# Performance work log

Measured on AMD Instinct MI355X. Metric: run time of the kernel, lower is better.

## Reference

```python
import jax, jax.numpy as jnp
import numpy as np

N_NODES = 100000
N_EDGES = 3200000
IN_DIM = 3
HID = 8
OUT_DIM = 1


def setup_inputs() -> dict:
    key = jax.random.key(0)
    ks = jax.random.split(key, 10)
    x = jax.random.normal(ks[0], (N_NODES, IN_DIM), dtype=jnp.float32)
    edge_index = jax.random.randint(ks[1], (2, N_EDGES), 0, N_NODES, dtype=jnp.int64)
    cat_dim = 2 * (HID + IN_DIM)  # 22
    s = lambda fan_in: 1.0 / np.sqrt(fan_in)
    W_in = jax.random.uniform(ks[2], (IN_DIM, HID), jnp.float32, -s(IN_DIM), s(IN_DIM))
    b_in = jnp.zeros((HID,), jnp.float32)
    W1 = jax.random.uniform(ks[3], (cat_dim, HID), jnp.float32, -s(cat_dim), s(cat_dim))
    b1 = jnp.zeros((HID,), jnp.float32)
    W2 = jax.random.uniform(ks[4], (HID, HID), jnp.float32, -s(HID), s(HID))
    b2 = jnp.zeros((HID,), jnp.float32)
    W_e = jax.random.uniform(ks[5], (cat_dim, OUT_DIM), jnp.float32, -s(cat_dim), s(cat_dim))
    b_e = jnp.zeros((OUT_DIM,), jnp.float32)
    return {"x": x, "edge_index": edge_index, "W_in": W_in, "b_in": b_in,
            "W1": W1, "b1": b1, "W2": W2, "b2": b2, "W_e": W_e, "b_e": b_e}


def reference(x, edge_index, W_in, b_in, W1, b1, W2, b2, W_e, b_e):
    src = edge_index[0]  # j (source)
    dst = edge_index[1]  # i (target)

    # inputnet: Linear + Tanh
    H = jnp.tanh(x @ W_in + b_in)               # [N, HID]
    feat = jnp.concatenate([H, x], axis=-1)      # [N, HID+IN_DIM]

    # One EdgeConv iteration (n_iters=1): message = nn(cat([x_i, x_j - x_i]))
    xi = feat[dst]                                # [E, 11]
    xj = feat[src]                                # [E, 11]
    e = jnp.concatenate([xi, xj - xi], axis=-1)   # [E, 22]
    m = jax.nn.sigmoid(e @ W1 + b1)               # [E, HID]
    m = jax.nn.sigmoid(m @ W2 + b2)               # [E, HID]
    H = jax.ops.segment_sum(m, dst, num_segments=N_NODES)  # scatter-add to targets
    feat = jnp.concatenate([H, x], axis=-1)       # [N, 11]

    # edgenetwork on concatenated endpoint features
    ef = jnp.concatenate([feat[src], feat[dst]], axis=-1)   # [E, 22]
    out = jax.nn.sigmoid(ef @ W_e + b_e)          # [E, 1]
    return out.squeeze(-1)                        # [E]
```

## Files before the change

kernel.cpp:

```cpp
#include <hip/hip_runtime.h>
#include <hip/hip_fp16.h>

#define TPB     256
#define BSH     9
#define BW      512
#define EPB     8192
#define NBMAX   256
#define MAXNB   1024
#define S_SPLIT 8
#define FXS     2097152.0f
#define FXSI    (1.0f / 2097152.0f)

static __device__ __forceinline__ float sigmoidf(float v) {
    return __builtin_amdgcn_rcpf(1.0f + __expf(-v));
}

static __device__ __forceinline__ void unpack8(uint4 u, float o[8]) {
    union { unsigned int u; __half2 h; } c0, c1, c2, c3;
    c0.u = u.x; c1.u = u.y; c2.u = u.z; c3.u = u.w;
    float2 f0 = __half22float2(c0.h), f1 = __half22float2(c1.h);
    float2 f2 = __half22float2(c2.h), f3 = __half22float2(c3.h);
    o[0]=f0.x; o[1]=f0.y; o[2]=f1.x; o[3]=f1.y;
    o[4]=f2.x; o[5]=f2.y; o[6]=f3.x; o[7]=f3.y;
}

__global__ void k_feat(const float* __restrict__ x,
                       const float* __restrict__ W_in,
                       const float* __restrict__ b_in,
                       const float* __restrict__ W1,
                       const float* __restrict__ b1,
                       float* __restrict__ gi,
                       __half* __restrict__ gjh, int n_nodes) {
    int n = blockIdx.x * blockDim.x + threadIdx.x;
    if (n >= n_nodes) return;
    float x0 = x[3*n], x1 = x[3*n+1], x2 = x[3*n+2];
    float f[11];
#pragma unroll
    for (int c = 0; c < 8; ++c)
        f[c] = tanhf(b_in[c] + x0*W_in[c] + x1*W_in[8+c] + x2*W_in[16+c]);
    f[8] = x0; f[9] = x1; f[10] = x2;
    float giv[8], gjv[8];
#pragma unroll
    for (int h = 0; h < 8; ++h) {
        float vi = b1[h], vj = 0.0f;
#pragma unroll
        for (int k = 0; k < 11; ++k) {
            float wa = W1[k*8+h], wb = W1[(11+k)*8+h];
            vi += f[k] * (wa - wb);
            vj += f[k] * wb;
        }
        giv[h] = vi; gjv[h] = vj;
    }
    float4* gip = (float4*)(gi + (size_t)n * 8);
    gip[0] = make_float4(giv[0], giv[1], giv[2], giv[3]);
    gip[1] = make_float4(giv[4], giv[5], giv[6], giv[7]);
    __align__(16) __half hj[8];
#pragma unroll
    for (int k = 0; k < 8; ++k) hj[k] = __float2half_rn(gjv[k]);
    *(uint4*)(gjh + (size_t)n * 8) = *(const uint4*)hj;
}

__global__ void k_hist2(const int* __restrict__ dst, int* __restrict__ raw,
                        int n_edges, int NB) {
    __shared__ int cnt[NBMAX];
    for (int b = threadIdx.x; b < NB; b += blockDim.x) cnt[b] = 0;
    __syncthreads();
    int e0 = blockIdx.x * EPB;
#pragma unroll
    for (int k = 0; k < EPB / (TPB * 4); ++k) {
        int e = e0 + k * TPB * 4 + threadIdx.x * 4;
        if (e + 3 < n_edges) {
            int4 d4 = *(const int4*)(dst + e);
            atomicAdd(&cnt[d4.x >> BSH], 1);
            atomicAdd(&cnt[d4.y >> BSH], 1);
            atomicAdd(&cnt[d4.z >> BSH], 1);
            atomicAdd(&cnt[d4.w >> BSH], 1);
        } else {
            int qe = min(e + 4, n_edges);
            for (int q = e; q < qe; ++q)
                atomicAdd(&cnt[dst[q] >> BSH], 1);
        }
    }
    __syncthreads();
    for (int b = threadIdx.x; b < NB; b += blockDim.x)
        raw[(size_t)blockIdx.x * NB + b] = cnt[b];
}

__global__ void k_scan_cols(const int* __restrict__ raw, int* __restrict__ rel,
                            int* __restrict__ totals, int NB, int NBLK) {
    __shared__ int s[TPB];
    int b = blockIdx.x, t = threadIdx.x;
    int carry = 0;
    for (int q = 0; q < NBLK; q += TPB) {
        int blk = q + t;
        int v = (blk < NBLK) ? raw[(size_t)blk * NB + b] : 0;
        __syncthreads();
        s[t] = v; __syncthreads();
        for (int o = 1; o < TPB; o <<= 1) {
            int u = (t >= o) ? s[t - o] : 0;
            __syncthreads();
            s[t] += u;
            __syncthreads();
        }
        if (blk < NBLK) rel[(size_t)blk * NB + b] = carry + s[t] - v;
        carry += s[TPB - 1];
    }
    if (t == 0) totals[b] = carry;
}

__global__ void k_base(const int* __restrict__ totals, int* __restrict__ base,
                       int NB) {
    __shared__ int s[MAXNB];
    int t = threadIdx.x;
    int v = (t < NB) ? ((totals[t] + 3) & ~3) : 0;
    s[t] = v; __syncthreads();
    for (int o = 1; o < MAXNB; o <<= 1) {
        int u = (t >= o) ? s[t - o] : 0;
        __syncthreads();
        s[t] += u;
        __syncthreads();
    }
    if (t < NB) base[t] = s[t] - v;
}

__launch_bounds__(TPB)
__global__ void k_scatter(const int* __restrict__ src, const int* __restrict__ dst,
                          const int* __restrict__ raw, const int* __restrict__ rel,
                          const int* __restrict__ base,
                          int* __restrict__ sorted, int n_edges, int NB) {
    __shared__ int stage[EPB];
    __shared__ int cnt[NBMAX];
    __shared__ int lscan[NBMAX];
    __shared__ int gd[NBMAX];
    __shared__ int s[TPB];
    int t = threadIdx.x;

    int carry = 0;
    for (int q0 = 0; q0 < NB; q0 += TPB) {
        int idx = q0 + t;
        int v = (idx < NB) ? raw[(size_t)blockIdx.x * NB + idx] : 0;
        __syncthreads();
        s[t] = v; __syncthreads();
        for (int o = 1; o < TPB; o <<= 1) {
            int u = (t >= o) ? s[t - o] : 0;
            __syncthreads();
            s[t] += u;
            __syncthreads();
        }
        if (idx < NB) lscan[idx] = carry + s[t] - v;
        carry += s[TPB - 1];
        __syncthreads();
    }
    for (int b = t; b < NB; b += TPB) {
        cnt[b] = lscan[b];
        gd[b]  = base[b] + rel[(size_t)blockIdx.x * NB + b];
    }
    __syncthreads();

    int e0 = blockIdx.x * EPB;
#pragma unroll
    for (int k = 0; k < EPB / (TPB * 4); ++k) {
        int e = e0 + k * TPB * 4 + t * 4;
        if (e + 3 < n_edges) {
            int4 s4 = *(const int4*)(src + e);
            int4 d4 = *(const int4*)(dst + e);
            int p;
            p = atomicAdd(&cnt[d4.x >> BSH], 1); stage[p] = (s4.x << BSH) | (d4.x & (BW-1));
            p = atomicAdd(&cnt[d4.y >> BSH], 1); stage[p] = (s4.y << BSH) | (d4.y & (BW-1));
            p = atomicAdd(&cnt[d4.z >> BSH], 1); stage[p] = (s4.z << BSH) | (d4.z & (BW-1));
            p = atomicAdd(&cnt[d4.w >> BSH], 1); stage[p] = (s4.w << BSH) | (d4.w & (BW-1));
        } else {
            int qe = min(e + 4, n_edges);
            for (int q = e; q < qe; ++q) {
                int d = dst[q];
                int p = atomicAdd(&cnt[d >> BSH], 1);
                stage[p] = (src[q] << BSH) | (d & (BW - 1));
            }
        }
    }
    __syncthreads();

    int wid = t >> 6, lane = t & 63;
    for (int b = wid; b < NB; b += (TPB / 64)) {
        int ls = lscan[b];
        int le = cnt[b];
        int g0 = gd[b];
        for (int i = ls + lane; i < le; i += 64)
            sorted[g0 + (i - ls)] = stage[i];
    }
}

__launch_bounds__(TPB, 4)
__global__ void k_bucket(const int* __restrict__ sorted, const int* __restrict__ base,
                         const int* __restrict__ totals,
                         const float* __restrict__ gi, const __half* __restrict__ gjh,
                         const float* __restrict__ W2, const float* __restrict__ b2,
                         const float* __restrict__ W_e,
                         float* __restrict__ part, int n_nodes, int NB, int NBP) {
    __shared__ int sa[BW], sc[BW];
    int t = threadIdx.x;
    int sl = blockIdx.x / NBP;
    int b  = blockIdx.x - sl * NBP;
    if (b >= NB) return;

    int nb0 = b * BW;
    for (int i = t; i < BW; i += TPB) { sa[i] = 0; sc[i] = 0; }
    __syncthreads();

    int beg = base[b];
    int len = totals[b];
    int qs = (((len + S_SPLIT - 1) / S_SPLIT) + 3) & ~3;
    int s0 = beg + sl * qs;
    int s1 = min(beg + len, s0 + qs);

    for (int g = s0 + t * 4; g < s1; g += TPB * 4) {
        if (g + 4 <= s1) {
            int4 pp = *(const int4*)(sorted + g);
            int d[4]  = { pp.x & (BW-1), pp.y & (BW-1), pp.z & (BW-1), pp.w & (BW-1) };
            int sj[4] = { pp.x >> BSH,   pp.y >> BSH,   pp.z >> BSH,   pp.w >> BSH };
            float ej[4][8];
#pragma unroll
            for (int q = 0; q < 4; ++q)
                unpack8(*(const uint4*)(gjh + (size_t)sj[q] * 8), ej[q]);
            float m[4][8];
#pragma unroll
            for (int q = 0; q < 4; ++q) {
                const float4* ip = (const float4*)(gi + (size_t)(nb0 + d[q]) * 8);
                float4 A = ip[0], B = ip[1];
                float ei[8] = {A.x,A.y,A.z,A.w,B.x,B.y,B.z,B.w};
#pragma unroll
                for (int k = 0; k < 8; ++k)
                    m[q][k] = sigmoidf(ei[k] + ej[q][k]);
            }
            float pa[4] = {0,0,0,0}, pc[4] = {0,0,0,0};
#pragma unroll
            for (int h = 0; h < 8; ++h) {
                float bb = b2[h];
                float v[4] = {bb, bb, bb, bb};
#pragma unroll
                for (int k = 0; k < 8; ++k) {
                    float w = W2[k*8+h];
#pragma unroll
                    for (int q = 0; q < 4; ++q) v[q] += m[q][k] * w;
                }
                float wa = W_e[h], wc = W_e[11+h];
#pragma unroll
                for (int q = 0; q < 4; ++q) {
                    float z = sigmoidf(v[q]);
                    pa[q] += z * wa; pc[q] += z * wc;
                }
            }
#pragma unroll
            for (int q = 0; q < 4; ++q) {
                atomicAdd(&sa[d[q]], __float2int_rn(pa[q] * FXS));
                atomicAdd(&sc[d[q]], __float2int_rn(pc[q] * FXS));
            }
        } else {
            for (int e = g; e < s1; ++e) {
                int p = sorted[e];
                int dl = p & (BW - 1);
                float ej[8];
                unpack8(*(const uint4*)(gjh + (size_t)(p >> BSH) * 8), ej);
                const float4* ip = (const float4*)(gi + (size_t)(nb0 + dl) * 8);
                float4 A = ip[0], B = ip[1];
                float ei[8] = {A.x,A.y,A.z,A.w,B.x,B.y,B.z,B.w};
                float m[8];
#pragma unroll
                for (int k = 0; k < 8; ++k) m[k] = sigmoidf(ei[k] + ej[k]);
                float pa = 0, pc = 0;
#pragma unroll
                for (int h = 0; h < 8; ++h) {
                    float v = b2[h];
#pragma unroll
                    for (int k = 0; k < 8; ++k) v += m[k] * W2[k*8+h];
                    float z = sigmoidf(v);
                    pa += z * W_e[h]; pc += z * W_e[11+h];
                }
                atomicAdd(&sa[dl], __float2int_rn(pa * FXS));
                atomicAdd(&sc[dl], __float2int_rn(pc * FXS));
            }
        }
    }
    __syncthreads();
    size_t row = (size_t)blockIdx.x * (2 * BW);
    for (int i = t; i < BW; i += TPB) {
        part[row + i]      = (float)sa[i] * FXSI;
        part[row + BW + i] = (float)sc[i] * FXSI;
    }
}

__global__ void k_acc(const float* __restrict__ part, const float* __restrict__ x,
                      const float* __restrict__ W_e, float* __restrict__ ac,
                      int n_nodes, int NBP) {
    int n = blockIdx.x * blockDim.x + threadIdx.x;
    if (n >= n_nodes) return;
    int b = n >> BSH, r = n & (BW - 1);
    float a = 0.0f, c = 0.0f;
#pragma unroll
    for (int s = 0; s < S_SPLIT; ++s) {
        const float* pp = part + ((size_t)(s * NBP + b)) * (2 * BW);
        a += pp[r];
        c += pp[BW + r];
    }
    float x0 = x[3*n], x1 = x[3*n+1], x2 = x[3*n+2];
    a += x0 * W_e[8]  + x1 * W_e[9]  + x2 * W_e[10];
    c += x0 * W_e[19] + x1 * W_e[20] + x2 * W_e[21];
    ac[2*n]     = a;
    ac[2*n + 1] = c;
}

__global__ void k_out2(const int* __restrict__ src, const int* __restrict__ dst,
                       const float* __restrict__ ac, const float* __restrict__ b_e,
                       float* __restrict__ out, int n_edges) {
    float bb = b_e[0];
    int e = (blockIdx.x * blockDim.x + threadIdx.x) * 4;
    if (e + 3 < n_edges) {
        int4 s4 = *(const int4*)(src + e);
        int4 d4 = *(const int4*)(dst + e);
        float4 o;
        o.x = sigmoidf(ac[2*s4.x] + ac[2*d4.x + 1] + bb);
        o.y = sigmoidf(ac[2*s4.y] + ac[2*d4.y + 1] + bb);
        o.z = sigmoidf(ac[2*s4.z] + ac[2*d4.z + 1] + bb);
        o.w = sigmoidf(ac[2*s4.w] + ac[2*d4.w + 1] + bb);
        *(float4*)(out + e) = o;
    } else {
        for (int q = e; q < n_edges; ++q)
            out[q] = sigmoidf(ac[2*src[q]] + ac[2*dst[q] + 1] + bb);
    }
}

__global__ void k_nodes(const float* __restrict__ x, const float* __restrict__ W_in,
                        const float* __restrict__ b_in, float* __restrict__ feat,
                        float* __restrict__ H2, int n_nodes) {
    int i = blockIdx.x * blockDim.x + threadIdx.x;
    if (i >= n_nodes) return;
    float x0 = x[3*i], x1 = x[3*i+1], x2 = x[3*i+2];
    float h[8];
#pragma unroll
    for (int c = 0; c < 8; ++c)
        h[c] = tanhf(b_in[c] + x0*W_in[c] + x1*W_in[8+c] + x2*W_in[16+c]);
    float4* fp = (float4*)(feat + (size_t)i * 12);
    fp[0] = make_float4(h[0],h[1],h[2],h[3]);
    fp[1] = make_float4(h[4],h[5],h[6],h[7]);
    fp[2] = make_float4(x0,x1,x2,0.0f);
    float4* hp = (float4*)(H2 + (size_t)i * 8);
    hp[0] = make_float4(0,0,0,0); hp[1] = make_float4(0,0,0,0);
}

__global__ void k_edges(const int* __restrict__ src, const int* __restrict__ dst,
                        const float* __restrict__ feat, const float* __restrict__ W1,
                        const float* __restrict__ b1, const float* __restrict__ W2,
                        const float* __restrict__ b2, float* __restrict__ H2,
                        int n_edges) {
    __shared__ float sW1[176], sW2[64], sb1[8], sb2[8];
    for (int t = threadIdx.x; t < 176; t += blockDim.x) sW1[t] = W1[t];
    for (int t = threadIdx.x; t < 64;  t += blockDim.x) sW2[t] = W2[t];
    if (threadIdx.x < 8) { sb1[threadIdx.x]=b1[threadIdx.x]; sb2[threadIdx.x]=b2[threadIdx.x]; }
    __syncthreads();
    int e = blockIdx.x * blockDim.x + threadIdx.x;
    if (e >= n_edges) return;
    int j = src[e], i = dst[e];
    const float4* fi = (const float4*)(feat + (size_t)i * 12);
    const float4* fj = (const float4*)(feat + (size_t)j * 12);
    float4 i0=fi[0],i1=fi[1],i2=fi[2],j0=fj[0],j1=fj[1],j2=fj[2];
    float xi[11]={i0.x,i0.y,i0.z,i0.w,i1.x,i1.y,i1.z,i1.w,i2.x,i2.y,i2.z};
    float xj[11]={j0.x,j0.y,j0.z,j0.w,j1.x,j1.y,j1.z,j1.w,j2.x,j2.y,j2.z};
    float dd[11];
#pragma unroll
    for (int k = 0; k < 11; ++k) dd[k]=xj[k]-xi[k];
    float m[8];
#pragma unroll
    for (int h = 0; h < 8; ++h) {
        float v = sb1[h];
#pragma unroll
        for (int k = 0; k < 11; ++k) v += xi[k]*sW1[k*8+h];
#pragma unroll
        for (int k = 0; k < 11; ++k) v += dd[k]*sW1[(11+k)*8+h];
        m[h] = sigmoidf(v);
    }
    float m2[8];
#pragma unroll
    for (int h = 0; h < 8; ++h) {
        float v = sb2[h];
#pragma unroll
        for (int k = 0; k < 8; ++k) v += m[k]*sW2[k*8+h];
        m2[h] = sigmoidf(v);
    }
    float* hp = H2 + (size_t)i * 8;
#pragma unroll
    for (int h = 0; h < 8; ++h) atomicAdd(hp + h, m2[h]);
}

__global__ void k_out(const int* __restrict__ src, const int* __restrict__ dst,
                      const float* __restrict__ H2, const float* __restrict__ x,
                      const float* __restrict__ W_e, const float* __restrict__ b_e,
                      float* __restrict__ out, int n_edges) {
    __shared__ float sW[22]; __shared__ float sb;
    if (threadIdx.x < 22) sW[threadIdx.x] = W_e[threadIdx.x];
    if (threadIdx.x == 0) sb = b_e[0];
    __syncthreads();
    int e = blockIdx.x * blockDim.x + threadIdx.x;
    if (e >= n_edges) return;
    int j = src[e], i = dst[e];
    const float4* hj = (const float4*)(H2 + (size_t)j * 8);
    const float4* hi = (const float4*)(H2 + (size_t)i * 8);
    float4 a0=hj[0],a1=hj[1],c0=hi[0],c1=hi[1];
    float acc = sb;
    acc += a0.x*sW[0]+a0.y*sW[1]+a0.z*sW[2]+a0.w*sW[3];
    acc += a1.x*sW[4]+a1.y*sW[5]+a1.z*sW[6]+a1.w*sW[7];
    acc += x[3*(size_t)j]*sW[8]+x[3*(size_t)j+1]*sW[9]+x[3*(size_t)j+2]*sW[10];
    acc += c0.x*sW[11]+c0.y*sW[12]+c0.z*sW[13]+c0.w*sW[14];
    acc += c1.x*sW[15]+c1.y*sW[16]+c1.z*sW[17]+c1.w*sW[18];
    acc += x[3*(size_t)i]*sW[19]+x[3*(size_t)i+1]*sW[20]+x[3*(size_t)i+2]*sW[21];
    out[e] = sigmoidf(acc);
}

extern "C" void kernel_launch(void* const* d_in, const int* in_sizes, int n_in,
                              void* d_out, int out_size, void* d_ws, size_t ws_size,
                              hipStream_t stream) {
    const float* x    = (const float*)d_in[0];
    const int*   ei   = (const int*)d_in[1];
    const float* W_in = (const float*)d_in[2];
    const float* b_in = (const float*)d_in[3];
    const float* W1   = (const float*)d_in[4];
    const float* b1   = (const float*)d_in[5];
    const float* W2   = (const float*)d_in[6];
    const float* b2   = (const float*)d_in[7];
    const float* W_e  = (const float*)d_in[8];
    const float* b_e  = (const float*)d_in[9];

    const int n_nodes = in_sizes[0] / 3;
    const int n_edges = in_sizes[1] / 2;
    const int* src = ei;
    const int* dst = ei + n_edges;
    float* out = (float*)d_out;

    const int NB   = (n_nodes + BW - 1) >> BSH;
    const int NBP  = (NB + 7) & ~7;
    const int NBLK = (n_edges + EPB - 1) / EPB;

    size_t off = 0;
    auto carve = [&](size_t bytes) { size_t o = off; off += (bytes + 255) & ~(size_t)255; return o; };
    char* ws = (char*)d_ws;
    size_t o_gi     = carve((size_t)n_nodes * 8 * 4);
    size_t o_gjh    = carve((size_t)n_nodes * 8 * 2);
    size_t o_ac     = carve((size_t)n_nodes * 2 * 4);
    size_t o_raw    = carve((size_t)NBLK * NB * 4);
    size_t o_rel    = carve((size_t)NBLK * NB * 4);
    size_t o_totals = carve((size_t)NB * 4);
    size_t o_base   = carve(((size_t)NB + 1) * 4);
    size_t o_sorted = carve(((size_t)n_edges + 4 * NBMAX) * 4);
    size_t o_part   = carve((size_t)NBP * S_SPLIT * 2 * BW * 4);
    bool fast = (off <= ws_size) && (NB <= NBMAX);

    if (fast) {
        float*  gi     = (float*)(ws + o_gi);
        __half* gjh    = (__half*)(ws + o_gjh);
        float*  ac     = (float*)(ws + o_ac);
        int*    raw    = (int*)(ws + o_raw);
        int*    rel    = (int*)(ws + o_rel);
        int*    totals = (int*)(ws + o_totals);
        int*    base   = (int*)(ws + o_base);
        int*    sorted = (int*)(ws + o_sorted);
        float*  part   = (float*)(ws + o_part);

        k_feat     <<<(n_nodes + TPB - 1) / TPB, TPB, 0, stream>>>(x, W_in, b_in, W1, b1, gi, gjh, n_nodes);
        k_hist2    <<<NBLK, TPB, 0, stream>>>(dst, raw, n_edges, NB);
        k_scan_cols<<<NB, TPB, 0, stream>>>(raw, rel, totals, NB, NBLK);
        k_base     <<<1, MAXNB, 0, stream>>>(totals, base, NB);
        k_scatter  <<<NBLK, TPB, 0, stream>>>(src, dst, raw, rel, base, sorted, n_edges, NB);
        k_bucket   <<<NBP * S_SPLIT, TPB, 0, stream>>>(sorted, base, totals, gi, gjh, W2, b2, W_e,
                                                       part, n_nodes, NB, NBP);
        k_acc      <<<(n_nodes + TPB - 1) / TPB, TPB, 0, stream>>>(part, x, W_e, ac, n_nodes, NBP);
        k_out2     <<<(n_edges / 4 + TPB - 1) / TPB + 1, TPB, 0, stream>>>(src, dst, ac, b_e, out, n_edges);
    } else {
        float* feat = (float*)d_ws;
        float* H2   = feat + (size_t)n_nodes * 12;
        k_nodes<<<(n_nodes + TPB - 1) / TPB, TPB, 0, stream>>>(x, W_in, b_in, feat, H2, n_nodes);
        k_edges<<<(n_edges + TPB - 1) / TPB, TPB, 0, stream>>>(src, dst, feat, W1, b1, W2, b2, H2, n_edges);
        k_out  <<<(n_edges + TPB - 1) / TPB, TPB, 0, stream>>>(src, dst, H2, x, W_e, b_e, out, n_edges);
    }
}
```

Measured before the change: 109.8 us.

## Double the destination bucket width and software-prefetch the next gather in k_bucket

New measurement: 111.2 us. Within noise of the previous version (+1.3%).

```diff
diff --git a/kernel.cpp b/kernel.cpp
--- a/kernel.cpp
+++ b/kernel.cpp
@@ -2,11 +2,10 @@
 #include <hip/hip_fp16.h>
 
 #define TPB     256
-#define BSH     9
-#define BW      512
+#define BSH     10
+#define BW      1024
 #define EPB     8192
-#define NBMAX   256
-#define MAXNB   1024
+#define NBMAX   128
 #define S_SPLIT 8
 #define FXS     2097152.0f
 #define FXSI    (1.0f / 2097152.0f)
@@ -110,11 +109,11 @@
 
 __global__ void k_base(const int* __restrict__ totals, int* __restrict__ base,
                        int NB) {
-    __shared__ int s[MAXNB];
+    __shared__ int s[NBMAX];
     int t = threadIdx.x;
     int v = (t < NB) ? ((totals[t] + 3) & ~3) : 0;
     s[t] = v; __syncthreads();
-    for (int o = 1; o < MAXNB; o <<= 1) {
+    for (int o = 1; o < NBMAX; o <<= 1) {
         int u = (t >= o) ? s[t - o] : 0;
         __syncthreads();
         s[t] += u;
@@ -135,11 +134,8 @@
     __shared__ int s[TPB];
     int t = threadIdx.x;
 
-    int carry = 0;
-    for (int q0 = 0; q0 < NB; q0 += TPB) {
-        int idx = q0 + t;
-        int v = (idx < NB) ? raw[(size_t)blockIdx.x * NB + idx] : 0;
-        __syncthreads();
+    {
+        int v = (t < NB) ? raw[(size_t)blockIdx.x * NB + t] : 0;
         s[t] = v; __syncthreads();
         for (int o = 1; o < TPB; o <<= 1) {
             int u = (t >= o) ? s[t - o] : 0;
@@ -147,10 +143,9 @@
             s[t] += u;
             __syncthreads();
         }
-        if (idx < NB) lscan[idx] = carry + s[t] - v;
-        carry += s[TPB - 1];
-        __syncthreads();
-    }
+        if (t < NB) lscan[t] = s[t] - v;
+    }
+    __syncthreads();
     for (int b = t; b < NB; b += TPB) {
         cnt[b] = lscan[b];
         gd[b]  = base[b] + rel[(size_t)blockIdx.x * NB + b];
@@ -213,72 +208,92 @@
     int s0 = beg + sl * qs;
     int s1 = min(beg + len, s0 + qs);
 
-    for (int g = s0 + t * 4; g < s1; g += TPB * 4) {
-        if (g + 4 <= s1) {
-            int4 pp = *(const int4*)(sorted + g);
-            int d[4]  = { pp.x & (BW-1), pp.y & (BW-1), pp.z & (BW-1), pp.w & (BW-1) };
-            int sj[4] = { pp.x >> BSH,   pp.y >> BSH,   pp.z >> BSH,   pp.w >> BSH };
-            float ej[4][8];
-#pragma unroll
-            for (int q = 0; q < 4; ++q)
-                unpack8(*(const uint4*)(gjh + (size_t)sj[q] * 8), ej[q]);
-            float m[4][8];
+    int g = s0 + t * 4;
+    bool v4 = (g + 4 <= s1);
+    int4 pp = make_int4(0,0,0,0);
+    uint4 uj[4];
+    if (v4) {
+        pp = *(const int4*)(sorted + g);
+        uj[0] = *(const uint4*)(gjh + (size_t)(pp.x >> BSH) * 8);
+        uj[1] = *(const uint4*)(gjh + (size_t)(pp.y >> BSH) * 8);
+        uj[2] = *(const uint4*)(gjh + (size_t)(pp.z >> BSH) * 8);
+        uj[3] = *(const uint4*)(gjh + (size_t)(pp.w >> BSH) * 8);
+    }
+    while (v4) {
+        int g2 = g + TPB * 4;
+        bool v4n = (g2 + 4 <= s1);
+        int4 pp2 = pp;
+        uint4 uj2[4] = { uj[0], uj[1], uj[2], uj[3] };
+        if (v4n) {
+            pp2 = *(const int4*)(sorted + g2);
+            uj2[0] = *(const uint4*)(gjh + (size_t)(pp2.x >> BSH) * 8);
+            uj2[1] = *(const uint4*)(gjh + (size_t)(pp2.y >> BSH) * 8);
+            uj2[2] = *(const uint4*)(gjh + (size_t)(pp2.z >> BSH) * 8);
+            uj2[3] = *(const uint4*)(gjh + (size_t)(pp2.w >> BSH) * 8);
+        }
+        int d[4] = { pp.x & (BW-1), pp.y & (BW-1), pp.z & (BW-1), pp.w & (BW-1) };
+        float ej[4][8];
+        unpack8(uj[0], ej[0]); unpack8(uj[1], ej[1]);
+        unpack8(uj[2], ej[2]); unpack8(uj[3], ej[3]);
+        float m[4][8];
+#pragma unroll
+        for (int q = 0; q < 4; ++q) {
+            const float4* ip = (const float4*)(gi + (size_t)(nb0 + d[q]) * 8);
+            float4 A = ip[0], B = ip[1];
+            float ei[8] = {A.x,A.y,A.z,A.w,B.x,B.y,B.z,B.w};
+#pragma unroll
+            for (int k = 0; k < 8; ++k)
+                m[q][k] = sigmoidf(ei[k] + ej[q][k]);
+        }
+        float pa[4] = {0,0,0,0}, pc[4] = {0,0,0,0};
+#pragma unroll
+        for (int h = 0; h < 8; ++h) {
+            float bb = b2[h];
+            float v[4] = {bb, bb, bb, bb};
+#pragma unroll
+            for (int k = 0; k < 8; ++k) {
+                float w = W2[k*8+h];
+#pragma unroll
+                for (int q = 0; q < 4; ++q) v[q] += m[q][k] * w;
+            }
+            float wa = W_e[h], wc = W_e[11+h];
 #pragma unroll
             for (int q = 0; q < 4; ++q) {
-                const float4* ip = (const float4*)(gi + (size_t)(nb0 + d[q]) * 8);
-                float4 A = ip[0], B = ip[1];
-                float ei[8] = {A.x,A.y,A.z,A.w,B.x,B.y,B.z,B.w};
-#pragma unroll
-                for (int k = 0; k < 8; ++k)
-                    m[q][k] = sigmoidf(ei[k] + ej[q][k]);
+                float z = sigmoidf(v[q]);
+                pa[q] += z * wa; pc[q] += z * wc;
             }
-            float pa[4] = {0,0,0,0}, pc[4] = {0,0,0,0};
+        }
+#pragma unroll
+        for (int q = 0; q < 4; ++q) {
+            atomicAdd(&sa[d[q]], __float2int_rn(pa[q] * FXS));
+            atomicAdd(&sc[d[q]], __float2int_rn(pc[q] * FXS));
+        }
+        pp = pp2; uj[0] = uj2[0]; uj[1] = uj2[1]; uj[2] = uj2[2]; uj[3] = uj2[3];
+        g = g2; v4 = v4n;
+    }
+    if (g < s1) {
+        for (int e = g; e < s1; ++e) {
+            int p = sorted[e];
+            int dl = p & (BW - 1);
+            float ej[8];
+            unpack8(*(const uint4*)(gjh + (size_t)(p >> BSH) * 8), ej);
+            const float4* ip = (const float4*)(gi + (size_t)(nb0 + dl) * 8);
+            float4 A = ip[0], B = ip[1];
+            float ei[8] = {A.x,A.y,A.z,A.w,B.x,B.y,B.z,B.w};
+            float m[8];
+#pragma unroll
+            for (int k = 0; k < 8; ++k) m[k] = sigmoidf(ei[k] + ej[k]);
+            float pa = 0, pc = 0;
 #pragma unroll
             for (int h = 0; h < 8; ++h) {
-                float bb = b2[h];
-                float v[4] = {bb, bb, bb, bb};
-#pragma unroll
-                for (int k = 0; k < 8; ++k) {
-                    float w = W2[k*8+h];
-#pragma unroll
-                    for (int q = 0; q < 4; ++q) v[q] += m[q][k] * w;
-                }
-                float wa = W_e[h], wc = W_e[11+h];
-#pragma unroll
-                for (int q = 0; q < 4; ++q) {
-                    float z = sigmoidf(v[q]);
-                    pa[q] += z * wa; pc[q] += z * wc;
-                }
+                float v = b2[h];
+#pragma unroll
+                for (int k = 0; k < 8; ++k) v += m[k] * W2[k*8+h];
+                float z = sigmoidf(v);
+                pa += z * W_e[h]; pc += z * W_e[11+h];
             }
-#pragma unroll
-            for (int q = 0; q < 4; ++q) {
-                atomicAdd(&sa[d[q]], __float2int_rn(pa[q] * FXS));
-                atomicAdd(&sc[d[q]], __float2int_rn(pc[q] * FXS));
-            }
-        } else {
-            for (int e = g; e < s1; ++e) {
-                int p = sorted[e];
-                int dl = p & (BW - 1);
-                float ej[8];
-                unpack8(*(const uint4*)(gjh + (size_t)(p >> BSH) * 8), ej);
-                const float4* ip = (const float4*)(gi + (size_t)(nb0 + dl) * 8);
-                float4 A = ip[0], B = ip[1];
-                float ei[8] = {A.x,A.y,A.z,A.w,B.x,B.y,B.z,B.w};
-                float m[8];
-#pragma unroll
-                for (int k = 0; k < 8; ++k) m[k] = sigmoidf(ei[k] + ej[k]);
-                float pa = 0, pc = 0;
-#pragma unroll
-                for (int h = 0; h < 8; ++h) {
-                    float v = b2[h];
-#pragma unroll
-                    for (int k = 0; k < 8; ++k) v += m[k] * W2[k*8+h];
-                    float z = sigmoidf(v);
-                    pa += z * W_e[h]; pc += z * W_e[11+h];
-                }
-                atomicAdd(&sa[dl], __float2int_rn(pa * FXS));
-                atomicAdd(&sc[dl], __float2int_rn(pc * FXS));
-            }
+            atomicAdd(&sa[dl], __float2int_rn(pa * FXS));
+            atomicAdd(&sc[dl], __float2int_rn(pc * FXS));
         }
     }
     __syncthreads();
@@ -467,7 +482,7 @@
         k_feat     <<<(n_nodes + TPB - 1) / TPB, TPB, 0, stream>>>(x, W_in, b_in, W1, b1, gi, gjh, n_nodes);
         k_hist2    <<<NBLK, TPB, 0, stream>>>(dst, raw, n_edges, NB);
         k_scan_cols<<<NB, TPB, 0, stream>>>(raw, rel, totals, NB, NBLK);
-        k_base     <<<1, MAXNB, 0, stream>>>(totals, base, NB);
+        k_base     <<<1, NBMAX, 0, stream>>>(totals, base, NB);
         k_scatter  <<<NBLK, TPB, 0, stream>>>(src, dst, raw, rel, base, sorted, n_edges, NB);
         k_bucket   <<<NBP * S_SPLIT, TPB, 0, stream>>>(sorted, base, totals, gi, gjh, W2, b2, W_e,
                                                        part, n_nodes, NB, NBP);
```

## Fuse node-feature and histogram kernels, inline base scan, double bucket split

Applied to the files above, without the earlier changes.

Result: faster. 103.8 us (-5.5%).

```diff
diff --git a/kernel.cpp b/kernel.cpp
--- a/kernel.cpp
+++ b/kernel.cpp
@@ -6,8 +6,7 @@
 #define BW      512
 #define EPB     8192
 #define NBMAX   256
-#define MAXNB   1024
-#define S_SPLIT 8
+#define S_SPLIT 16
 #define FXS     2097152.0f
 #define FXSI    (1.0f / 2097152.0f)
 
@@ -24,66 +23,69 @@
     o[4]=f2.x; o[5]=f2.y; o[6]=f3.x; o[7]=f3.y;
 }
 
-__global__ void k_feat(const float* __restrict__ x,
+__global__ void k_prep(const float* __restrict__ x,
                        const float* __restrict__ W_in,
                        const float* __restrict__ b_in,
                        const float* __restrict__ W1,
                        const float* __restrict__ b1,
                        float* __restrict__ gi,
-                       __half* __restrict__ gjh, int n_nodes) {
-    int n = blockIdx.x * blockDim.x + threadIdx.x;
-    if (n >= n_nodes) return;
-    float x0 = x[3*n], x1 = x[3*n+1], x2 = x[3*n+2];
-    float f[11];
-#pragma unroll
-    for (int c = 0; c < 8; ++c)
-        f[c] = tanhf(b_in[c] + x0*W_in[c] + x1*W_in[8+c] + x2*W_in[16+c]);
-    f[8] = x0; f[9] = x1; f[10] = x2;
-    float giv[8], gjv[8];
-#pragma unroll
-    for (int h = 0; h < 8; ++h) {
-        float vi = b1[h], vj = 0.0f;
-#pragma unroll
-        for (int k = 0; k < 11; ++k) {
-            float wa = W1[k*8+h], wb = W1[(11+k)*8+h];
-            vi += f[k] * (wa - wb);
-            vj += f[k] * wb;
-        }
-        giv[h] = vi; gjv[h] = vj;
-    }
-    float4* gip = (float4*)(gi + (size_t)n * 8);
-    gip[0] = make_float4(giv[0], giv[1], giv[2], giv[3]);
-    gip[1] = make_float4(giv[4], giv[5], giv[6], giv[7]);
-    __align__(16) __half hj[8];
-#pragma unroll
-    for (int k = 0; k < 8; ++k) hj[k] = __float2half_rn(gjv[k]);
-    *(uint4*)(gjh + (size_t)n * 8) = *(const uint4*)hj;
-}
-
-__global__ void k_hist2(const int* __restrict__ dst, int* __restrict__ raw,
-                        int n_edges, int NB) {
+                       __half* __restrict__ gjh,
+                       const int* __restrict__ dst,
+                       int* __restrict__ raw,
+                       int n_nodes, int n_edges, int NB, int NBLK) {
     __shared__ int cnt[NBMAX];
-    for (int b = threadIdx.x; b < NB; b += blockDim.x) cnt[b] = 0;
-    __syncthreads();
-    int e0 = blockIdx.x * EPB;
-#pragma unroll
-    for (int k = 0; k < EPB / (TPB * 4); ++k) {
-        int e = e0 + k * TPB * 4 + threadIdx.x * 4;
-        if (e + 3 < n_edges) {
-            int4 d4 = *(const int4*)(dst + e);
-            atomicAdd(&cnt[d4.x >> BSH], 1);
-            atomicAdd(&cnt[d4.y >> BSH], 1);
-            atomicAdd(&cnt[d4.z >> BSH], 1);
-            atomicAdd(&cnt[d4.w >> BSH], 1);
-        } else {
-            int qe = min(e + 4, n_edges);
-            for (int q = e; q < qe; ++q)
-                atomicAdd(&cnt[dst[q] >> BSH], 1);
-        }
-    }
-    __syncthreads();
-    for (int b = threadIdx.x; b < NB; b += blockDim.x)
-        raw[(size_t)blockIdx.x * NB + b] = cnt[b];
+    int t = threadIdx.x;
+    if ((int)blockIdx.x < NBLK) {
+        for (int b = t; b < NB; b += TPB) cnt[b] = 0;
+        __syncthreads();
+        int e0 = blockIdx.x * EPB;
+#pragma unroll
+        for (int k = 0; k < EPB / (TPB * 4); ++k) {
+            int e = e0 + k * TPB * 4 + t * 4;
+            if (e + 3 < n_edges) {
+                int4 d4 = *(const int4*)(dst + e);
+                atomicAdd(&cnt[d4.x >> BSH], 1);
+                atomicAdd(&cnt[d4.y >> BSH], 1);
+                atomicAdd(&cnt[d4.z >> BSH], 1);
+                atomicAdd(&cnt[d4.w >> BSH], 1);
+            } else {
+                int qe = min(e + 4, n_edges);
+                for (int q = e; q < qe; ++q)
+                    atomicAdd(&cnt[dst[q] >> BSH], 1);
+            }
+        }
+        __syncthreads();
+        for (int b = t; b < NB; b += TPB)
+            raw[(size_t)blockIdx.x * NB + b] = cnt[b];
+    } else {
+        int n = ((int)blockIdx.x - NBLK) * TPB + t;
+        if (n >= n_nodes) return;
+        float x0 = x[3*n], x1 = x[3*n+1], x2 = x[3*n+2];
+        float f[11];
+#pragma unroll
+        for (int c = 0; c < 8; ++c)
+            f[c] = tanhf(b_in[c] + x0*W_in[c] + x1*W_in[8+c] + x2*W_in[16+c]);
+        f[8] = x0; f[9] = x1; f[10] = x2;
+        float giv[8], gjv[8];
+#pragma unroll
+        for (int h = 0; h < 8; ++h) {
+            float vi = b1[h], vj = 0.0f;
+#pragma unroll
+            for (int k = 0; k < 11; ++k) {
+                float wa = W1[k*8+h], wb = W1[(11+k)*8+h];
+                vi += f[k] * (wa - wb);
+                vj += f[k] * wb;
+            }
+            giv[h] = vi; gjv[h] = vj;
+        }
+        float4* gip = (float4*)(gi + (size_t)n * 8);
+        gip[0] = make_float4(giv[0], giv[1], giv[2], giv[3]);
+        gip[1] = make_float4(giv[4], giv[5], giv[6], giv[7]);
+        __align__(16) __half hj[8];
+#pragma unroll
+        for (int k = 0; k < 8; ++k) hj[k] = __float2half_rn(gjv[k]);
+        *(uint4*)(gjh + (size_t)n * 8) = *(const uint4*)hj;
+    }
 }
 
 __global__ void k_scan_cols(const int* __restrict__ raw, int* __restrict__ rel,
@@ -108,37 +110,37 @@
     if (t == 0) totals[b] = carry;
 }
 
-__global__ void k_base(const int* __restrict__ totals, int* __restrict__ base,
-                       int NB) {
-    __shared__ int s[MAXNB];
-    int t = threadIdx.x;
+static __device__ __forceinline__ void base_scan(const int* __restrict__ totals,
+                                                 int* s, int* sbase, int NB, int t) {
     int v = (t < NB) ? ((totals[t] + 3) & ~3) : 0;
     s[t] = v; __syncthreads();
-    for (int o = 1; o < MAXNB; o <<= 1) {
+    for (int o = 1; o < TPB; o <<= 1) {
         int u = (t >= o) ? s[t - o] : 0;
         __syncthreads();
         s[t] += u;
         __syncthreads();
     }
-    if (t < NB) base[t] = s[t] - v;
+    if (t < NB) sbase[t] = s[t] - v;
+    __syncthreads();
 }
 
 __launch_bounds__(TPB)
 __global__ void k_scatter(const int* __restrict__ src, const int* __restrict__ dst,
                           const int* __restrict__ raw, const int* __restrict__ rel,
-                          const int* __restrict__ base,
+                          const int* __restrict__ totals,
                           int* __restrict__ sorted, int n_edges, int NB) {
     __shared__ int stage[EPB];
     __shared__ int cnt[NBMAX];
     __shared__ int lscan[NBMAX];
     __shared__ int gd[NBMAX];
+    __shared__ int sbase[NBMAX];
     __shared__ int s[TPB];
     int t = threadIdx.x;
 
-    int carry = 0;
-    for (int q0 = 0; q0 < NB; q0 += TPB) {
-        int idx = q0 + t;
-        int v = (idx < NB) ? raw[(size_t)blockIdx.x * NB + idx] : 0;
+    base_scan(totals, s, sbase, NB, t);
+
+    {
+        int v = (t < NB) ? raw[(size_t)blockIdx.x * NB + t] : 0;
         __syncthreads();
         s[t] = v; __syncthreads();
         for (int o = 1; o < TPB; o <<= 1) {
@@ -147,13 +149,11 @@
             s[t] += u;
             __syncthreads();
         }
-        if (idx < NB) lscan[idx] = carry + s[t] - v;
-        carry += s[TPB - 1];
-        __syncthreads();
-    }
-    for (int b = t; b < NB; b += TPB) {
-        cnt[b] = lscan[b];
-        gd[b]  = base[b] + rel[(size_t)blockIdx.x * NB + b];
+        if (t < NB) {
+            lscan[t] = s[t] - v;
+            cnt[t]   = s[t] - v;
+            gd[t]    = sbase[t] + rel[(size_t)blockIdx.x * NB + t];
+        }
     }
     __syncthreads();
 
@@ -191,23 +191,27 @@
 }
 
 __launch_bounds__(TPB, 4)
-__global__ void k_bucket(const int* __restrict__ sorted, const int* __restrict__ base,
+__global__ void k_bucket(const int* __restrict__ sorted,
                          const int* __restrict__ totals,
                          const float* __restrict__ gi, const __half* __restrict__ gjh,
                          const float* __restrict__ W2, const float* __restrict__ b2,
                          const float* __restrict__ W_e,
                          float* __restrict__ part, int n_nodes, int NB, int NBP) {
     __shared__ int sa[BW], sc[BW];
+    __shared__ int sbase[NBMAX];
+    __shared__ int s[TPB];
     int t = threadIdx.x;
     int sl = blockIdx.x / NBP;
     int b  = blockIdx.x - sl * NBP;
+
+    base_scan(totals, s, sbase, NB, t);
     if (b >= NB) return;
 
     int nb0 = b * BW;
     for (int i = t; i < BW; i += TPB) { sa[i] = 0; sc[i] = 0; }
     __syncthreads();
 
-    int beg = base[b];
+    int beg = sbase[b];
     int len = totals[b];
     int qs = (((len + S_SPLIT - 1) / S_SPLIT) + 3) & ~3;
     int s0 = beg + sl * qs;
@@ -438,6 +442,7 @@
     const int NB   = (n_nodes + BW - 1) >> BSH;
     const int NBP  = (NB + 7) & ~7;
     const int NBLK = (n_edges + EPB - 1) / EPB;
+    const int NFB  = (n_nodes + TPB - 1) / TPB;
 
     size_t off = 0;
     auto carve = [&](size_t bytes) { size_t o = off; off += (bytes + 255) & ~(size_t)255; return o; };
@@ -448,7 +453,6 @@
     size_t o_raw    = carve((size_t)NBLK * NB * 4);
     size_t o_rel    = carve((size_t)NBLK * NB * 4);
     size_t o_totals = carve((size_t)NB * 4);
-    size_t o_base   = carve(((size_t)NB + 1) * 4);
     size_t o_sorted = carve(((size_t)n_edges + 4 * NBMAX) * 4);
     size_t o_part   = carve((size_t)NBP * S_SPLIT * 2 * BW * 4);
     bool fast = (off <= ws_size) && (NB <= NBMAX);
@@ -460,16 +464,14 @@
         int*    raw    = (int*)(ws + o_raw);
         int*    rel    = (int*)(ws + o_rel);
         int*    totals = (int*)(ws + o_totals);
-        int*    base   = (int*)(ws + o_base);
         int*    sorted = (int*)(ws + o_sorted);
         float*  part   = (float*)(ws + o_part);
 
-        k_feat     <<<(n_nodes + TPB - 1) / TPB, TPB, 0, stream>>>(x, W_in, b_in, W1, b1, gi, gjh, n_nodes);
-        k_hist2    <<<NBLK, TPB, 0, stream>>>(dst, raw, n_edges, NB);
+        k_prep     <<<NBLK + NFB, TPB, 0, stream>>>(x, W_in, b_in, W1, b1, gi, gjh,
+                                                    dst, raw, n_nodes, n_edges, NB, NBLK);
         k_scan_cols<<<NB, TPB, 0, stream>>>(raw, rel, totals, NB, NBLK);
-        k_base     <<<1, MAXNB, 0, stream>>>(totals, base, NB);
-        k_scatter  <<<NBLK, TPB, 0, stream>>>(src, dst, raw, rel, base, sorted, n_edges, NB);
-        k_bucket   <<<NBP * S_SPLIT, TPB, 0, stream>>>(sorted, base, totals, gi, gjh, W2, b2, W_e,
+        k_scatter  <<<NBLK, TPB, 0, stream>>>(src, dst, raw, rel, totals, sorted, n_edges, NB);
+        k_bucket   <<<NBP * S_SPLIT, TPB, 0, stream>>>(sorted, totals, gi, gjh, W2, b2, W_e,
                                                        part, n_nodes, NB, NBP);
         k_acc      <<<(n_nodes + TPB - 1) / TPB, TPB, 0, stream>>>(part, x, W_e, ac, n_nodes, NBP);
         k_out2     <<<(n_edges / 4 + TPB - 1) / TPB + 1, TPB, 0, stream>>>(src, dst, ac, b_e, out, n_edges);
```
